# Kernel optimization log

Measured on AMD Instinct MI355X. Metric: run time of the kernel, lower is better.

Reference implementation:

```python
import jax, jax.numpy as jnp
import numpy as np

SCALE_H, SCALE_W = 160.0, 160.0  # init spatial_scale
ALIGNED = False


def setup_inputs() -> dict:
    key = jax.random.key(0)
    k1, k2, k3 = jax.random.split(key, 3)
    feats = jax.random.normal(k1, (4, 256, 160, 160), dtype=jnp.float32)
    B, N = 4, 512
    bidx = jax.random.randint(k2, (N,), 0, B).astype(jnp.float32)
    p = jax.random.uniform(k3, (N, 4), dtype=jnp.float32)
    x1 = p[:, 0] * 0.7
    y1 = p[:, 1] * 0.7
    x2 = x1 + 0.05 + p[:, 2] * 0.25
    y2 = y1 + 0.05 + p[:, 3] * 0.25
    rois = jnp.stack([bidx, x1, y1, x2, y2], axis=1)
    return {
        "input_images_or_features": feats,
        "rois": rois,
        "output_height": 14,
        "output_width": 14,
    }


def reference(input_images_or_features, rois, output_height, output_width):
    feats = input_images_or_features  # [B, C, H, W]
    B, C, H, W = feats.shape
    OH, OW = int(output_height), int(output_width)
    dt = rois.dtype

    b = rois[:, 0].astype(jnp.int32)                      # [N]
    x1 = rois[:, 1] * SCALE_W
    y1 = rois[:, 2] * SCALE_H
    x2 = rois[:, 3] * SCALE_W
    y2 = rois[:, 4] * SCALE_H
    rw = x2 - x1
    rh = y2 - y1

    xs = jnp.arange(OW, dtype=dt) / max(OW - 1, 1)
    ys = jnp.arange(OH, dtype=dt) / max(OH - 1, 1)
    gy, gx = jnp.meshgrid(ys, xs, indexing="ij")          # [OH, OW]

    fx = x1[:, None, None] + gx[None] * rw[:, None, None]  # [N, OH, OW]
    fy = y1[:, None, None] + gy[None] * rh[:, None, None]

    if ALIGNED:
        nfx = fx / (W - 1) * 2 - 1
        nfy = fy / (H - 1) * 2 - 1
        ix = (nfx + 1) / 2 * (W - 1)
        iy = (nfy + 1) / 2 * (H - 1)
    else:
        nfx = fx / W * 2 - 1
        nfy = fy / H * 2 - 1
        ix = ((nfx + 1) * W - 1) / 2
        iy = ((nfy + 1) * H - 1) / 2

    x0f = jnp.floor(ix)
    y0f = jnp.floor(iy)
    x0 = x0f.astype(jnp.int32)
    y0 = y0f.astype(jnp.int32)

    wx1 = ix - x0f   # weight for x0+1
    wx0 = 1.0 - wx1
    wy1 = iy - y0f
    wy0 = 1.0 - wy1

    bb = b[:, None, None]

    def corner(yi, xi, w):
        valid = (xi >= 0) & (xi < W) & (yi >= 0) & (yi < H)
        xc = jnp.clip(xi, 0, W - 1)
        yc = jnp.clip(yi, 0, H - 1)
        v = feats[bb, :, yc, xc]                 # [N, OH, OW, C]
        return v * (w * valid.astype(dt))[..., None]

    out = (corner(y0, x0, wy0 * wx0)
           + corner(y0, x0 + 1, wy0 * wx1)
           + corner(y0 + 1, x0, wy1 * wx0)
           + corner(y0 + 1, x0 + 1, wy1 * wx1))   # [N, OH, OW, C]
    return jnp.transpose(out, (0, 3, 1, 2))       # [N, C, OH, OW]
```

## Files before the change

kernel.cpp:

```cpp
#include <hip/hip_runtime.h>
#include <cstddef>
#include <cstdint>

#define RA_C   256
#define RA_H   160
#define RA_W   160
#define RA_OH  14
#define RA_OW  14
#define RA_S   196
#define RA_SCALE 160.0f

#define CQ     16
#define NCQ    (RA_C / CQ)
#define NBIN   (4 * RA_H)
#define MAXE   128
#define CHUNK  48
#define ROW_F  164
#define CH_F   332

struct XParam { int p; float w0, w1; };

__device__ __forceinline__ XParam axis_param(float lo, float ext, int o,
                                             float inv, int lim)
{
    float g   = (float)o * inv;
    float f   = lo + g * ext;
    float nf  = f / (float)lim * 2.0f - 1.0f;
    float ix  = ((nf + 1.0f) * (float)lim - 1.0f) * 0.5f;
    float i0f = floorf(ix);
    int   i0  = (int)i0f;
    float w1  = ix - i0f, w0 = 1.0f - w1;
    bool  v0  = (i0 >= 0) && (i0 < lim);
    int   ip  = i0 + 1;
    bool  v1  = (ip >= 0) && (ip < lim);
    float W0  = w0 * (v0 ? 1.0f : 0.0f);
    float W1  = w1 * (v1 ? 1.0f : 0.0f);
    int   p   = min(max(i0, 0), lim - 2);
    bool  swp = (i0 != p);
    XParam r;
    r.p  = p;
    r.w0 = swp ? W1 : W0;
    r.w1 = swp ? W0 : W1;
    return r;
}

__global__ __launch_bounds__(256) void roi_prep_kernel(
    const float* __restrict__ rois,
    float4* __restrict__ xq,
    int2*   __restrict__ xp,
    float2* __restrict__ yw,
    int* __restrict__ counts, unsigned short* __restrict__ entries, int N)
{
    int t = blockIdx.x * 256 + (int)threadIdx.x;
    if (t >= N * RA_OH) return;
    int n = t / RA_OH, i = t - n * RA_OH;
    const float* r = rois + (size_t)n * 5;
    int   b  = (int)r[0];
    float x1 = r[1] * RA_SCALE;
    float y1 = r[2] * RA_SCALE;
    float rw = r[3] * RA_SCALE - x1;
    float rh = r[4] * RA_SCALE - y1;

    XParam yp = axis_param(y1, rh, i, 1.0f / (RA_OH - 1), RA_H);
    yw[t] = make_float2(yp.w0, yp.w1);
    int bin = b * RA_H + yp.p;
    int pos = atomicAdd(&counts[bin], 1);
    if (pos < MAXE)
        entries[(size_t)bin * MAXE + pos] = (unsigned short)((n << 4) | i);

    if (i < RA_OW / 2) {
        XParam xa = axis_param(x1, rw, 2 * i,     1.0f / (RA_OW - 1), RA_W);
        XParam xb = axis_param(x1, rw, 2 * i + 1, 1.0f / (RA_OW - 1), RA_W);
        xq[n * 7 + i] = make_float4(xa.w0, xa.w1, xb.w0, xb.w1);
        xp[n * 7 + i] = make_int2(xa.p, xb.p);
    }
}

__global__ __launch_bounds__(256) void roi_main_kernel(
    const float* __restrict__ feats, float* __restrict__ out,
    const float4* __restrict__ xq, const int2* __restrict__ xp,
    const float2* __restrict__ yw,
    const int* __restrict__ counts, const unsigned short* __restrict__ entries)
{
    __shared__ __align__(16) float win[CQ * CH_F];
    __shared__ int    s_ent[CHUNK];
    __shared__ float2 s_wy[CHUNK];
    __shared__ __align__(16) float4 s_xw[CHUNK][7];
    __shared__ int2   s_xi[CHUNK][7];

    constexpr int HW = RA_H * RA_W;

    int bid = blockIdx.x;
    int cq  = bid & (NCQ - 1);
    int bin = bid >> 4;
    int cnt = counts[bin];
    if (cnt == 0) return;
    if (cnt > MAXE) cnt = MAXE;
    int b = bin / RA_H;
    int p = bin - b * RA_H;
    int tid = (int)threadIdx.x;
    int c0 = cq * CQ;

    const float* fb = feats + (((size_t)b * RA_C + c0) * RA_H + p) * RA_W;
    for (int i = tid; i < CQ * 2 * (RA_W / 4); i += 256) {
        int c   = i / 80;
        int rem = i - c * 80;
        int row = rem / 40;
        int x4  = rem - row * 40;
        float4 v = *(const float4*)(fb + (size_t)c * HW + row * RA_W + x4 * 4);
        *(float4*)&win[c * CH_F + row * ROW_F + x4 * 4] = v;
    }

    int half = tid & 127;
    int par  = tid >> 7;
    int c  = half / 7;
    int j  = half - c * 7;
    bool geo = half < CQ * 7;
    int oofs = (c0 + c) * RA_S + 2 * j;
    const unsigned short* el = entries + (size_t)bin * MAXE;
    const float* wc = &win[c * CH_F];

    for (int base = 0; base < cnt; base += CHUNK) {
        int m = min(CHUNK, cnt - base);

        if (base) __syncthreads();
        if (tid < m) {
            int ent = el[base + tid];
            s_ent[tid] = ent;
            int n = ent >> 4;
            s_wy[tid] = yw[n * RA_OH + (ent & 15)];
#pragma unroll
            for (int jj = 0; jj < 7; ++jj) {
                s_xw[tid][jj] = xq[n * 7 + jj];
                s_xi[tid][jj] = xp[n * 7 + jj];
            }
        }
        __syncthreads();

        for (int e = 0; e < m; e += 2) {
            int idx = e + par;
            bool act = geo && (idx < m);
            int ent = __builtin_amdgcn_readfirstlane(s_ent[idx]);
            int n = ent >> 4, oy = ent & 15;
            float2 wy = s_wy[idx];
            if (act) {
                float4 xw = s_xw[idx][j];
                int2   xi = s_xi[idx][j];
                const float* pa = wc + xi.x;
                const float* pb = wc + xi.y;
                float p00 = pa[0],     p01 = pa[1];
                float p10 = pa[ROW_F], p11 = pa[ROW_F + 1];
                float q00 = pb[0],     q01 = pb[1];
                float q10 = pb[ROW_F], q11 = pb[ROW_F + 1];

                float a0 = wy.x * xw.x, b0 = wy.x * xw.y;
                float a1 = wy.y * xw.x, b1 = wy.y * xw.y;
                float v0 = fmaf(a0, p00, fmaf(b0, p01, fmaf(a1, p10, b1 * p11)));
                float c0w = wy.x * xw.z, d0 = wy.x * xw.w;
                float c1w = wy.y * xw.z, d1 = wy.y * xw.w;
                float v1 = fmaf(c0w, q00, fmaf(d0, q01, fmaf(c1w, q10, d1 * q11)));

                float* ob = out + ((size_t)n * RA_C * RA_S + oy * RA_OW + oofs);
                *(float2*)ob = make_float2(v0, v1);
            }
        }
    }
}

__device__ __forceinline__ float2 ldg_f2(const float* p) {
    float2 r;
    __builtin_memcpy(&r, p, sizeof(float2));
    return r;
}

__global__ __launch_bounds__(256) void roi_align_fallback(
    const float* __restrict__ feats, const float* __restrict__ rois,
    float* __restrict__ out, int N, int bpc)
{
    constexpr int S   = RA_OH * RA_OW;
    constexpr int K   = 8;
    constexpr int CG  = RA_C / K;
    constexpr int CGX = CG / 8;
    constexpr int HW  = RA_H * RA_W;

    int bid   = blockIdx.x;
    int xcd   = bid & 7;
    int local = bid >> 3;
    int cg    = xcd * CGX + local / bpc;
    int rem   = local - (local / bpc) * bpc;
    int idx_in_cg = rem * 256 + (int)threadIdx.x;
    if (idx_in_cg >= N * S) return;
    int n = idx_in_cg / S;
    int s = idx_in_cg - n * S;
    int oy = s / RA_OW;
    int ox = s - oy * RA_OW;

    const float* r = rois + (size_t)n * 5;
    int   b  = (int)r[0];
    float x1 = r[1] * RA_SCALE;
    float y1 = r[2] * RA_SCALE;
    float rw = r[3] * RA_SCALE - x1;
    float rh = r[4] * RA_SCALE - y1;
    XParam xpr = axis_param(x1, rw, ox, 1.0f / (RA_OW - 1), RA_W);
    XParam ypr = axis_param(y1, rh, oy, 1.0f / (RA_OH - 1), RA_H);
    float a0 = ypr.w0 * xpr.w0, b0 = ypr.w0 * xpr.w1;
    float a1 = ypr.w1 * xpr.w0, b1 = ypr.w1 * xpr.w1;
    int o0 = ypr.p * RA_W + xpr.p;
    int o1 = o0 + RA_W;

    int c0 = cg * K;
    const float* fbp = feats + ((size_t)b * RA_C + c0) * HW;
    float*       op  = out   + ((size_t)n * RA_C + c0) * S + s;
#pragma unroll
    for (int k = 0; k < K; ++k) {
        const float* f = fbp + (size_t)k * HW;
        float2 p0 = ldg_f2(f + o0);
        float2 p1 = ldg_f2(f + o1);
        float v = fmaf(a0, p0.x, fmaf(b0, p0.y, fmaf(a1, p1.x, b1 * p1.y)));
        op[(size_t)k * S] = v;
    }
}

extern "C" void kernel_launch(void* const* d_in, const int* in_sizes, int n_in,
                              void* d_out, int out_size, void* d_ws, size_t ws_size,
                              hipStream_t stream) {
    const float* feats = (const float*)d_in[0];
    const float* rois  = (const float*)d_in[1];
    float*       out   = (float*)d_out;

    int N = in_sizes[1] / 5;

    size_t off_xp  = (size_t)N * 7 * 16;
    size_t off_yw  = off_xp + (size_t)N * 7 * 8;
    size_t off_cnt = off_yw + (size_t)N * 14 * 8;
    size_t off_ent = off_cnt + (size_t)NBIN * 4;
    size_t need    = off_ent + (size_t)NBIN * MAXE * 2;

    if (d_ws != nullptr && ws_size >= need && N <= 512) {
        char* ws = (char*)d_ws;
        float4* xq = (float4*)ws;
        int2*   xp = (int2*)(ws + off_xp);
        float2* yw = (float2*)(ws + off_yw);
        int*    counts = (int*)(ws + off_cnt);
        unsigned short* entries = (unsigned short*)(ws + off_ent);

        hipMemsetAsync(counts, 0, NBIN * sizeof(int), stream);
        int gridA = (N * RA_OH + 255) / 256;
        roi_prep_kernel<<<gridA, 256, 0, stream>>>(rois, xq, xp, yw,
                                                   counts, entries, N);
        roi_main_kernel<<<NBIN * NCQ, 256, 0, stream>>>(feats, out, xq, xp, yw,
                                                        counts, entries);
    } else {
        constexpr int S = RA_OH * RA_OW;
        int bpc  = (N * S + 255) / 256;
        int grid = (RA_C / 8) * bpc;
        roi_align_fallback<<<grid, 256, 0, stream>>>(feats, rois, out, N, bpc);
    }
}
```

Before: 219.4 us.

## Load ROI params per thread from global with software prefetch instead of LDS staging

Removes the per-chunk LDS staging of y-weights and x-params, leaving only the entry list in shared memory. Each thread now loads its own params from global (L2-cached) and prefetches the next entry's params one iteration ahead. This cuts LDS usage and a serial staging phase. It also shrinks CHUNK and adds a waves-per-EU launch bound to raise occupancy. The cost is more redundant global loads per thread and higher register pressure.

```diff
diff --git a/kernel.cpp b/kernel.cpp
--- a/kernel.cpp
+++ b/kernel.cpp
@@ -14,7 +14,7 @@
 #define NCQ    (RA_C / CQ)
 #define NBIN   (4 * RA_H)
 #define MAXE   128
-#define CHUNK  48
+#define CHUNK  32
 #define ROW_F  164
 #define CH_F   332
 
@@ -76,17 +76,29 @@
     }
 }
 
-__global__ __launch_bounds__(256) void roi_main_kernel(
+struct Prm { int ent; float2 wy; float4 xw; int2 xi; };
+
+__device__ __forceinline__ Prm load_prm(int ent, int j,
+    const float4* __restrict__ xq, const int2* __restrict__ xp,
+    const float2* __restrict__ yw)
+{
+    Prm p;
+    p.ent = ent;
+    int n = ent >> 4;
+    p.wy = yw[n * RA_OH + (ent & 15)];
+    p.xw = xq[n * 7 + j];
+    p.xi = xp[n * 7 + j];
+    return p;
+}
+
+__global__ __launch_bounds__(256, 7) void roi_main_kernel(
     const float* __restrict__ feats, float* __restrict__ out,
     const float4* __restrict__ xq, const int2* __restrict__ xp,
     const float2* __restrict__ yw,
     const int* __restrict__ counts, const unsigned short* __restrict__ entries)
 {
     __shared__ __align__(16) float win[CQ * CH_F];
-    __shared__ int    s_ent[CHUNK];
-    __shared__ float2 s_wy[CHUNK];
-    __shared__ __align__(16) float4 s_xw[CHUNK][7];
-    __shared__ int2   s_xi[CHUNK][7];
+    __shared__ int s_ent[CHUNK];
 
     constexpr int HW = RA_H * RA_W;
 
@@ -124,45 +136,37 @@
         int m = min(CHUNK, cnt - base);
 
         if (base) __syncthreads();
-        if (tid < m) {
-            int ent = el[base + tid];
-            s_ent[tid] = ent;
-            int n = ent >> 4;
-            s_wy[tid] = yw[n * RA_OH + (ent & 15)];
-#pragma unroll
-            for (int jj = 0; jj < 7; ++jj) {
-                s_xw[tid][jj] = xq[n * 7 + jj];
-                s_xi[tid][jj] = xp[n * 7 + jj];
-            }
-        }
+        if (tid < m) s_ent[tid] = el[base + tid];
         __syncthreads();
 
+        Prm cur = load_prm(s_ent[min(par, m - 1)], j, xq, xp, yw);
         for (int e = 0; e < m; e += 2) {
+            int ipre = min(e + 2 + par, m - 1);
+            Prm nxt = load_prm(s_ent[ipre], j, xq, xp, yw);
+
             int idx = e + par;
             bool act = geo && (idx < m);
-            int ent = __builtin_amdgcn_readfirstlane(s_ent[idx]);
+            int ent = __builtin_amdgcn_readfirstlane(cur.ent);
             int n = ent >> 4, oy = ent & 15;
-            float2 wy = s_wy[idx];
             if (act) {
-                float4 xw = s_xw[idx][j];
-                int2   xi = s_xi[idx][j];
-                const float* pa = wc + xi.x;
-                const float* pb = wc + xi.y;
+                const float* pa = wc + cur.xi.x;
+                const float* pb = wc + cur.xi.y;
                 float p00 = pa[0],     p01 = pa[1];
                 float p10 = pa[ROW_F], p11 = pa[ROW_F + 1];
                 float q00 = pb[0],     q01 = pb[1];
                 float q10 = pb[ROW_F], q11 = pb[ROW_F + 1];
 
-                float a0 = wy.x * xw.x, b0 = wy.x * xw.y;
-                float a1 = wy.y * xw.x, b1 = wy.y * xw.y;
+                float a0 = cur.wy.x * cur.xw.x, b0 = cur.wy.x * cur.xw.y;
+                float a1 = cur.wy.y * cur.xw.x, b1 = cur.wy.y * cur.xw.y;
                 float v0 = fmaf(a0, p00, fmaf(b0, p01, fmaf(a1, p10, b1 * p11)));
-                float c0w = wy.x * xw.z, d0 = wy.x * xw.w;
-                float c1w = wy.y * xw.z, d1 = wy.y * xw.w;
+                float c0w = cur.wy.x * cur.xw.z, d0 = cur.wy.x * cur.xw.w;
+                float c1w = cur.wy.y * cur.xw.z, d1 = cur.wy.y * cur.xw.w;
                 float v1 = fmaf(c0w, q00, fmaf(d0, q01, fmaf(c1w, q10, d1 * q11)));
 
                 float* ob = out + ((size_t)n * RA_C * RA_S + oy * RA_OW + oofs);
                 *(float2*)ob = make_float2(v0, v1);
             }
+            cur = nxt;
         }
     }
 }
```

Result: slower. 233.2 us (+6.3%).

## Load only the x-range of feature rows actually touched per bin

Applied to the files above, without the earlier changes.

The prep kernel now records per-bin minimum and maximum x indices touched by all ROIs via atomicMin/atomicMax. The main kernel uses these to load only that aligned column span of the two feature rows into shared memory, with a wave-per-row copy loop, instead of the full 160-wide rows. This is meant to cut global memory reads for bins whose ROIs cover a narrow horizontal range. It also halves CHUNK and adds a min-blocks occupancy hint to launch_bounds, and it costs an extra memset plus extra atomics in prep.

```diff
diff --git a/kernel.cpp b/kernel.cpp
--- a/kernel.cpp
+++ b/kernel.cpp
@@ -14,7 +14,7 @@
 #define NCQ    (RA_C / CQ)
 #define NBIN   (4 * RA_H)
 #define MAXE   128
-#define CHUNK  48
+#define CHUNK  24
 #define ROW_F  164
 #define CH_F   332
 
@@ -49,7 +49,8 @@
     float4* __restrict__ xq,
     int2*   __restrict__ xp,
     float2* __restrict__ yw,
-    int* __restrict__ counts, unsigned short* __restrict__ entries, int N)
+    int* __restrict__ counts, int* __restrict__ xhi, int* __restrict__ xlo,
+    unsigned short* __restrict__ entries, int N)
 {
     int t = blockIdx.x * 256 + (int)threadIdx.x;
     if (t >= N * RA_OH) return;
@@ -68,6 +69,11 @@
     if (pos < MAXE)
         entries[(size_t)bin * MAXE + pos] = (unsigned short)((n << 4) | i);
 
+    int lo = axis_param(x1, rw, 0,         1.0f / (RA_OW - 1), RA_W).p;
+    int hi = axis_param(x1, rw, RA_OW - 1, 1.0f / (RA_OW - 1), RA_W).p + 1;
+    atomicMin(&xlo[bin], lo);
+    atomicMax(&xhi[bin], hi);
+
     if (i < RA_OW / 2) {
         XParam xa = axis_param(x1, rw, 2 * i,     1.0f / (RA_OW - 1), RA_W);
         XParam xb = axis_param(x1, rw, 2 * i + 1, 1.0f / (RA_OW - 1), RA_W);
@@ -76,11 +82,12 @@
     }
 }
 
-__global__ __launch_bounds__(256) void roi_main_kernel(
+__global__ __launch_bounds__(256, 6) void roi_main_kernel(
     const float* __restrict__ feats, float* __restrict__ out,
     const float4* __restrict__ xq, const int2* __restrict__ xp,
     const float2* __restrict__ yw,
-    const int* __restrict__ counts, const unsigned short* __restrict__ entries)
+    const int* __restrict__ counts, const int* __restrict__ xhi,
+    const int* __restrict__ xlo, const unsigned short* __restrict__ entries)
 {
     __shared__ __align__(16) float win[CQ * CH_F];
     __shared__ int    s_ent[CHUNK];
@@ -101,14 +108,16 @@
     int tid = (int)threadIdx.x;
     int c0 = cq * CQ;
 
-    const float* fb = feats + (((size_t)b * RA_C + c0) * RA_H + p) * RA_W;
-    for (int i = tid; i < CQ * 2 * (RA_W / 4); i += 256) {
-        int c   = i / 80;
-        int rem = i - c * 80;
-        int row = rem / 40;
-        int x4  = rem - row * 40;
-        float4 v = *(const float4*)(fb + (size_t)c * HW + row * RA_W + x4 * 4);
-        *(float4*)&win[c * CH_F + row * ROW_F + x4 * 4] = v;
+    int xloA = xlo[bin] & ~3;
+    int nf4  = min(((xhi[bin] - xloA) >> 2) + 1, (RA_W - xloA) >> 2);
+    const float* fb = feats + (((size_t)b * RA_C + c0) * RA_H + p) * RA_W + xloA;
+    int wv = tid >> 6, lane = tid & 63;
+    for (int rc = wv; rc < CQ * 2; rc += 4) {
+        int c = rc >> 1, row = rc & 1;
+        const float* src = fb + (size_t)c * HW + row * RA_W;
+        float*       dst = &win[c * CH_F + row * ROW_F];
+        for (int m4 = lane; m4 < nf4; m4 += 64)
+            *(float4*)&dst[4 * m4] = *(const float4*)&src[4 * m4];
     }
 
     int half = tid & 127;
@@ -118,7 +127,7 @@
     bool geo = half < CQ * 7;
     int oofs = (c0 + c) * RA_S + 2 * j;
     const unsigned short* el = entries + (size_t)bin * MAXE;
-    const float* wc = &win[c * CH_F];
+    const float* wc = &win[c * CH_F] - xloA;
 
     for (int base = 0; base < cnt; base += CHUNK) {
         int m = min(CHUNK, cnt - base);
@@ -233,7 +242,9 @@
     size_t off_xp  = (size_t)N * 7 * 16;
     size_t off_yw  = off_xp + (size_t)N * 7 * 8;
     size_t off_cnt = off_yw + (size_t)N * 14 * 8;
-    size_t off_ent = off_cnt + (size_t)NBIN * 4;
+    size_t off_xhi = off_cnt + (size_t)NBIN * 4;
+    size_t off_xlo = off_xhi + (size_t)NBIN * 4;
+    size_t off_ent = off_xlo + (size_t)NBIN * 4;
     size_t need    = off_ent + (size_t)NBIN * MAXE * 2;
 
     if (d_ws != nullptr && ws_size >= need && N <= 512) {
@@ -242,14 +253,17 @@
         int2*   xp = (int2*)(ws + off_xp);
         float2* yw = (float2*)(ws + off_yw);
         int*    counts = (int*)(ws + off_cnt);
+        int*    xhi    = (int*)(ws + off_xhi);
+        int*    xlo    = (int*)(ws + off_xlo);
         unsigned short* entries = (unsigned short*)(ws + off_ent);
 
-        hipMemsetAsync(counts, 0, NBIN * sizeof(int), stream);
+        hipMemsetAsync(counts, 0, 2 * NBIN * sizeof(int), stream);
+        hipMemsetAsync(xlo, 0x7F, NBIN * sizeof(int), stream);
         int gridA = (N * RA_OH + 255) / 256;
         roi_prep_kernel<<<gridA, 256, 0, stream>>>(rois, xq, xp, yw,
-                                                   counts, entries, N);
+                                                   counts, xhi, xlo, entries, N);
         roi_main_kernel<<<NBIN * NCQ, 256, 0, stream>>>(feats, out, xq, xp, yw,
-                                                        counts, entries);
+                                                        counts, xhi, xlo, entries);
     } else {
         constexpr int S = RA_OH * RA_OW;
         int bpc  = (N * S + 255) / 256;
```

Result: slower. 233.3 us (+6.3%).
